# Kernel optimization log

Measured on AMD Instinct MI355X. Metric: run time of the kernel, lower is better.

## Reference

```python
import jax, jax.numpy as jnp
import numpy as np

S = 16384          # vision tokens (one image, 128x128 patches)
HID = 1280         # vision_hidden_size
H = 16             # num heads
D = HID // H       # head_dim = 80
L = 8              # vision_depth
FF = 3456          # vision_intermediate_size
WIN = 64           # tokens per attention window
UNIT = 4           # spatial_merge_size ** 2
OUT = 2048         # vision_out_hidden_size
PV = 3 * 2 * 16 * 16  # patch volume = 1536


def setup_inputs() -> dict:
    keys = iter(jax.random.split(jax.random.key(0), 32))
    def nrm(shape, fan_in):
        return jax.random.normal(next(keys), shape, jnp.float32) * (fan_in ** -0.5)
    ang = jax.random.uniform(next(keys), (S, D // 2), jnp.float32, 0.0, 2.0 * float(np.pi))
    ang = jnp.concatenate([ang, ang], axis=-1)  # rotate_half-compatible duplicated layout
    return {
        "x": jax.random.normal(next(keys), (S, PV), jnp.float32),
        "cos": jnp.cos(ang), "sin": jnp.sin(ang),
        "cu_seqlens": jnp.arange(S // WIN + 1, dtype=jnp.int32) * WIN,
        "pe_w": nrm((PV, HID), PV), "pe_b": jnp.zeros((HID,), jnp.float32),
        "ln1_w": jnp.ones((L, HID), jnp.float32), "ln1_b": jnp.zeros((L, HID), jnp.float32),
        "qkv_w": nrm((L, HID, 3 * HID), HID), "qkv_b": jnp.zeros((L, 3 * HID), jnp.float32),
        "proj_w": nrm((L, HID, HID), HID), "proj_b": jnp.zeros((L, HID), jnp.float32),
        "ln2_w": jnp.ones((L, HID), jnp.float32), "ln2_b": jnp.zeros((L, HID), jnp.float32),
        "fc1_w": nrm((L, HID, FF), HID), "fc1_b": jnp.zeros((L, FF), jnp.float32),
        "fc2_w": nrm((L, FF, HID), FF), "fc2_b": jnp.zeros((L, HID), jnp.float32),
        "m_ln_w": jnp.ones((HID,), jnp.float32), "m_ln_b": jnp.zeros((HID,), jnp.float32),
        "m_fc1_w": nrm((UNIT * HID, UNIT * HID), UNIT * HID), "m_fc1_b": jnp.zeros((UNIT * HID,), jnp.float32),
        "m_fc2_w": nrm((UNIT * HID, OUT), UNIT * HID), "m_fc2_b": jnp.zeros((OUT,), jnp.float32),
    }


def _ln(t, w, b, eps=1e-6):
    m = jnp.mean(t, axis=-1, keepdims=True)
    v = jnp.mean((t - m) ** 2, axis=-1, keepdims=True)
    return (t - m) * jax.lax.rsqrt(v + eps) * w + b


def _forward(cu_seqlens, x, cos, sin, pe_w, pe_b, ln1_w, ln1_b, qkv_w, qkv_b,
             proj_w, proj_b, ln2_w, ln2_b, fc1_w, fc1_b, fc2_w, fc2_b,
             m_ln_w, m_ln_b, m_fc1_w, m_fc1_b, m_fc2_w, m_fc2_b):
    NW = cu_seqlens.shape[0] - 1  # uniform windows (static)
    W = S // NW
    scale = D ** -0.5
    cosr = cos[:, None, :]  # [S,1,D]
    sinr = sin[:, None, :]

    def rope(t):  # t: [S,H,D]
        t1, t2 = jnp.split(t, 2, axis=-1)
        return t * cosr + jnp.concatenate((-t2, t1), axis=-1) * sinr

    h = x @ pe_w + pe_b  # patch embed: [S, HID]

    def block(h, p):
        l1w, l1b, qw, qb, pw, pb, l2w, l2b, f1w, f1b, f2w, f2b = p
        xn = _ln(h, l1w, l1b)
        q, k, v = jnp.split(xn @ qw + qb, 3, axis=-1)
        q = rope(q.reshape(S, H, D))
        k = rope(k.reshape(S, H, D))
        v = v.reshape(S, H, D)
        # block-diagonal (windowed) attention, fp32 scores as in source
        qw_ = q.reshape(NW, W, H, D)
        kw_ = k.reshape(NW, W, H, D)
        vw_ = v.reshape(NW, W, H, D)
        scores = jnp.einsum('wqhd,wkhd->whqk', qw_, kw_) * scale
        attn = jnp.einsum('whqk,wkhd->wqhd', jax.nn.softmax(scores, axis=-1), vw_)
        h = h + (attn.reshape(S, HID) @ pw + pb)
        xn2 = _ln(h, l2w, l2b)
        h = h + (jax.nn.gelu(xn2 @ f1w + f1b, approximate=True) @ f2w + f2b)
        return h, None

    h, _ = jax.lax.scan(block, h, (ln1_w, ln1_b, qkv_w, qkv_b, proj_w, proj_b,
                                   ln2_w, ln2_b, fc1_w, fc1_b, fc2_w, fc2_b))
    # patch merger (pre-shuffle norm)
    hm = _ln(h, m_ln_w, m_ln_b).reshape(-1, UNIT * HID)  # [S/4, 5120]
    return jax.nn.gelu(hm @ m_fc1_w + m_fc1_b, approximate=True) @ m_fc2_w + m_fc2_b


def reference(x, cos, sin, cu_seqlens, pe_w, pe_b, ln1_w, ln1_b, qkv_w, qkv_b,
              proj_w, proj_b, ln2_w, ln2_b, fc1_w, fc1_b, fc2_w, fc2_b,
              m_ln_w, m_ln_b, m_fc1_w, m_fc1_b, m_fc2_w, m_fc2_b):
    return _forward(cu_seqlens, x, cos, sin, pe_w, pe_b, ln1_w, ln1_b, qkv_w, qkv_b,
                    proj_w, proj_b, ln2_w, ln2_b, fc1_w, fc1_b, fc2_w, fc2_b,
                    m_ln_w, m_ln_b, m_fc1_w, m_fc1_b, m_fc2_w, m_fc2_b)
```

## Files before the change

kernel.cpp:

```cpp
#include <hip/hip_runtime.h>

typedef unsigned short ushortT;
typedef __attribute__((ext_vector_type(8))) short short8;
typedef __attribute__((ext_vector_type(8))) unsigned short ushort8;
typedef __attribute__((ext_vector_type(4))) unsigned short ushort4v;
typedef __attribute__((ext_vector_type(4))) float f32x4;

#define DEVINL __device__ __forceinline__

DEVINL ushortT f2bf(float f) {
    unsigned u = __builtin_bit_cast(unsigned, f);
    u += 0x7FFFu + ((u >> 16) & 1u);
    return (ushortT)(u >> 16);
}
DEVINL float bf2f(ushortT h) {
    unsigned u = ((unsigned)h) << 16;
    return __builtin_bit_cast(float, u);
}
DEVINL float gelu_tanh(float x) {
    float x3 = x * x * x;
    return 0.5f * x * (1.0f + tanhf(0.7978845608028654f * (x + 0.044715f * x3)));
}

#define GLOAD_LDS16(g, l)                                                     \
    __builtin_amdgcn_global_load_lds(                                         \
        (const __attribute__((address_space(1))) void*)(g),                   \
        (__attribute__((address_space(3))) void*)(l), 16, 0, 0)

#define WAITV(n) asm volatile("s_waitcnt vmcnt(" #n ")" ::: "memory")
#define MEMFENCE() asm volatile("" ::: "memory")
#define BAR() __builtin_amdgcn_s_barrier()
#define BARF() MEMFENCE(); BAR(); MEMFENCE()

__global__ __launch_bounds__(256) void cast_bf16_4(const float* __restrict__ in,
                                                   ushortT* __restrict__ out, long n4) {
    long i = (long)blockIdx.x * 256 + threadIdx.x;
    if (i < n4) {
        const float* p = in + i * 4;
        ushort4v o;
        o[0] = f2bf(p[0]); o[1] = f2bf(p[1]); o[2] = f2bf(p[2]); o[3] = f2bf(p[3]);
        ((ushort4v*)out)[i] = o;
    }
}

__global__ __launch_bounds__(256) void transpose_cast(const float* __restrict__ in,
                                                      ushortT* __restrict__ out,
                                                      int K, int N, int Npad) {
    __shared__ float tile[32][33];
    long zi = (long)blockIdx.z * K * N;
    long zo = (long)blockIdx.z * Npad * K;
    const float* ip = in + zi;
    ushortT* op = out + zo;
    int t = threadIdx.x, bx = blockIdx.x, by = blockIdx.y;
#pragma unroll
    for (int i = 0; i < 4; i++) {
        int idx = i * 256 + t, r = idx >> 5, c = idx & 31;
        int col = bx * 32 + c;
        tile[r][c] = (col < N) ? ip[(long)(by * 32 + r) * N + col] : 0.0f;
    }
    __syncthreads();
#pragma unroll
    for (int i = 0; i < 4; i++) {
        int idx = i * 256 + t, r = idx >> 5, c = idx & 31;
        op[(long)(bx * 32 + r) * K + by * 32 + c] = f2bf(tile[c][r]);
    }
}

__global__ __launch_bounds__(256) void pad_bias(const float* __restrict__ in,
                                                float* __restrict__ out,
                                                int n_in, int n_out, int total) {
    int i = blockIdx.x * 256 + threadIdx.x;
    if (i < total) {
        int l = i / n_out, c = i % n_out;
        out[i] = (c < n_in) ? in[l * n_in + c] : 0.0f;
    }
}

__global__ __launch_bounds__(256) void ln_to_bf16(const float* __restrict__ in,
                                                  const float* __restrict__ w,
                                                  const float* __restrict__ b,
                                                  ushortT* __restrict__ out) {
    const int row = blockIdx.x;
    const float* x = in + (long)row * 1280;
    __shared__ float red[4];
    float v[5];
    float s = 0.f;
#pragma unroll
    for (int i = 0; i < 5; i++) { v[i] = x[threadIdx.x + i * 256]; s += v[i]; }
#pragma unroll
    for (int o = 32; o > 0; o >>= 1) s += __shfl_xor(s, o);
    int wave = threadIdx.x >> 6;
    if ((threadIdx.x & 63) == 0) red[wave] = s;
    __syncthreads();
    float mean = (red[0] + red[1] + red[2] + red[3]) * (1.0f / 1280.0f);
    float q = 0.f;
#pragma unroll
    for (int i = 0; i < 5; i++) { float d = v[i] - mean; q += d * d; }
#pragma unroll
    for (int o = 32; o > 0; o >>= 1) q += __shfl_xor(q, o);
    __syncthreads();
    if ((threadIdx.x & 63) == 0) red[wave] = q;
    __syncthreads();
    float var = (red[0] + red[1] + red[2] + red[3]) * (1.0f / 1280.0f);
    float rs = rsqrtf(var + 1e-6f);
#pragma unroll
    for (int i = 0; i < 5; i++) {
        int c = threadIdx.x + i * 256;
        out[(long)row * 1280 + c] = f2bf((v[i] - mean) * rs * w[c] + b[c]);
    }
}


#define GSTAGE(mat, ls, base, ld, k0, buf)                                    \
    _Pragma("unroll") for (int j = 0; j < 2; j++) {                           \
        int c = j * 256 + t; int sr = c >> 2, sl = c & 3;                     \
        GLOAD_LDS16(mat + (base + sr) * ld + (k0) + ((sl ^ ((sr >> 1) & 3)) * 8), \
                    &ls[buf][c * 8]);                                         \
    }
#define GREAD()                                                               \
    _Pragma("unroll") for (int m = 0; m < 4; m++) {                           \
        int r = wr * 64 + m * 16 + lr;                                        \
        aF[m] = *(const short8*)&lsA[rbuf][r * 32 + ((lg ^ ((r >> 1) & 3)) * 8)]; \
    }                                                                         \
    _Pragma("unroll") for (int n = 0; n < 4; n++) {                           \
        int r = wc * 64 + n * 16 + lr;                                        \
        bF[n] = *(const short8*)&lsB[rbuf][r * 32 + ((lg ^ ((r >> 1) & 3)) * 8)]; \
    }
#define GMFMA()                                                               \
    __builtin_amdgcn_s_setprio(1);                                            \
    _Pragma("unroll") for (int m = 0; m < 4; m++)                             \
    _Pragma("unroll") for (int n = 0; n < 4; n++)                             \
        acc[m][n] = __builtin_amdgcn_mfma_f32_16x16x32_bf16(                  \
            aF[m], bF[n], acc[m][n], 0, 0, 0);                                \
    __builtin_amdgcn_s_setprio(0);

template <bool OBF, bool RES, bool GEL>
__global__ __launch_bounds__(256, 3)
void gemm_r3(const ushortT* __restrict__ A, const ushortT* __restrict__ Bt,
             const float* __restrict__ bias, const float* __restrict__ res,
             void* __restrict__ out, int M, int N, int K, int lda, int ldb) {
    __shared__ ushortT lsA[3][4096];
    __shared__ ushortT lsB[3][4096];
    const int t = threadIdx.x;
    const int lane = t & 63, lr = lane & 15, lg = lane >> 4;
    const int wave = t >> 6;
    const int wr = wave >> 1, wc = wave & 1;

    const int nwg = gridDim.x, orig = blockIdx.x;
    const int q = nwg >> 3, r8 = nwg & 7;
    const int xcd = orig & 7, loc = orig >> 3;
    const int wg = (xcd < r8 ? xcd * (q + 1) : r8 * (q + 1) + (xcd - r8) * q) + loc;
    const int gx = N >> 7;
    const size_t brow = (size_t)(wg / gx) * 128;
    const size_t bcol = (size_t)(wg % gx) * 128;

    f32x4 acc[4][4];
#pragma unroll
    for (int m = 0; m < 4; m++)
#pragma unroll
        for (int n = 0; n < 4; n++) acc[m][n] = f32x4{0.f, 0.f, 0.f, 0.f};

    GSTAGE(A, lsA, brow, lda, 0, 0);
    GSTAGE(Bt, lsB, bcol, ldb, 0, 0);
    GSTAGE(A, lsA, brow, lda, 32, 1);
    GSTAGE(Bt, lsB, bcol, ldb, 32, 1);
    WAITV(4); BARF();

    short8 aF[4], bF[4];
    const int NT = K >> 5;
    int tt = 0;
    for (; tt < NT - 2; ++tt) {
        const int rbuf = tt % 3, sbuf = (tt + 2) % 3;
        const int k2 = (tt + 2) << 5;
        MEMFENCE();
        GREAD();
        GSTAGE(A, lsA, brow, lda, k2, sbuf);
        GSTAGE(Bt, lsB, bcol, ldb, k2, sbuf);
        WAITV(4);
        BARF();
        GMFMA();
    }
    {
        const int rbuf = tt % 3;
        MEMFENCE();
        GREAD();
        WAITV(0);
        BARF();
        GMFMA();
        ++tt;
    }
    {
        const int rbuf = tt % 3;
        MEMFENCE();
        GREAD();
        GMFMA();
    }

#pragma unroll
    for (int m = 0; m < 4; m++) {
#pragma unroll
        for (int n = 0; n < 4; n++) {
#pragma unroll
            for (int rr = 0; rr < 4; rr++) {
                size_t row = brow + wr * 64 + m * 16 + lg * 4 + rr;
                size_t col = bcol + wc * 64 + n * 16 + lr;
                float v = acc[m][n][rr] + bias[col];
                if (RES) v += res[row * N + col];
                if (GEL) v = gelu_tanh(v);
                if (OBF) ((ushortT*)out)[row * N + col] = f2bf(v);
                else     ((float*)out)[row * N + col] = v;
            }
        }
    }
}

__global__ __launch_bounds__(256) void attn_win(const ushortT* __restrict__ qkv,
                                                const float* __restrict__ cosb,
                                                const float* __restrict__ sinb,
                                                ushortT* __restrict__ out) {
    const int w = blockIdx.x, h = blockIdx.y;
    __shared__ ushortT qs[64 * 96];
    __shared__ ushortT ks[64 * 96];
    __shared__ ushortT vt[80 * 80];
    __shared__ float   sc[64 * 65];
    __shared__ ushortT pb[64 * 80];
    const int t = threadIdx.x, wave = t >> 6, lane = t & 63, lr = lane & 15, lg = lane >> 4;
    const ushortT* bq = qkv + (long)w * 64 * 3840 + h * 80;

    for (int c = t; c < 640; c += 256) {
        int r = c / 10, cb = c % 10;
        const ushortT* qp = bq + (long)r * 3840;
        ushort8 qa = *(const ushort8*)(qp + cb * 8);
        ushort8 ka = *(const ushort8*)(qp + 1280 + cb * 8);
        int pcb = (cb < 5) ? cb + 5 : cb - 5;
        ushort8 qpr = *(const ushort8*)(qp + pcb * 8);
        ushort8 kpr = *(const ushort8*)(qp + 1280 + pcb * 8);
        long srow = (long)w * 64 + r;
        const float* cp = cosb + srow * 80 + cb * 8;
        const float* sp = sinb + srow * 80 + cb * 8;
        float sgn = (cb < 5) ? -1.f : 1.f;
        ushort8 qo, ko;
#pragma unroll
        for (int j = 0; j < 8; j++) {
            float c_ = cp[j], s_ = sp[j] * sgn;
            qo[j] = f2bf(bf2f(qa[j]) * c_ + bf2f(qpr[j]) * s_);
            ko[j] = f2bf(bf2f(ka[j]) * c_ + bf2f(kpr[j]) * s_);
        }
        *(ushort8*)&qs[r * 96 + cb * 8] = qo;
        *(ushort8*)&ks[r * 96 + cb * 8] = ko;
        ushort8 vv = *(const ushort8*)(qp + 2560 + cb * 8);
#pragma unroll
        for (int j = 0; j < 8; j++) vt[(cb * 8 + j) * 80 + r] = vv[j];
    }
    for (int idx = t; idx < 1024; idx += 256) {
        int r = idx >> 4, c2 = 80 + (idx & 15);
        qs[r * 96 + c2] = 0;
        ks[r * 96 + c2] = 0;
    }
    __syncthreads();

    f32x4 sa[4];
#pragma unroll
    for (int n = 0; n < 4; n++) sa[n] = f32x4{0.f, 0.f, 0.f, 0.f};
#pragma unroll
    for (int kk = 0; kk < 3; kk++) {
        short8 aq = *(const short8*)&qs[(wave * 16 + lr) * 96 + kk * 32 + lg * 8];
#pragma unroll
        for (int n = 0; n < 4; n++) {
            short8 bk = *(const short8*)&ks[(n * 16 + lr) * 96 + kk * 32 + lg * 8];
            sa[n] = __builtin_amdgcn_mfma_f32_16x16x32_bf16(aq, bk, sa[n], 0, 0, 0);
        }
    }
    const float scale = 0.11180339887498949f;
#pragma unroll
    for (int n = 0; n < 4; n++)
#pragma unroll
        for (int r = 0; r < 4; r++)
            sc[(wave * 16 + lg * 4 + r) * 65 + n * 16 + lr] = sa[n][r] * scale;
    __syncthreads();

    {
        int row = t >> 2, q4 = t & 3;
        float pv[16];
        float mx = -1e30f;
#pragma unroll
        for (int j = 0; j < 16; j++) { pv[j] = sc[row * 65 + q4 * 16 + j]; mx = fmaxf(mx, pv[j]); }
        mx = fmaxf(mx, __shfl_xor(mx, 1));
        mx = fmaxf(mx, __shfl_xor(mx, 2));
        float sum = 0.f;
#pragma unroll
        for (int j = 0; j < 16; j++) { pv[j] = __expf(pv[j] - mx); sum += pv[j]; }
        sum += __shfl_xor(sum, 1);
        sum += __shfl_xor(sum, 2);
        float inv = 1.0f / sum;
#pragma unroll
        for (int j = 0; j < 16; j++) pb[row * 80 + q4 * 16 + j] = f2bf(pv[j] * inv);
    }
    __syncthreads();

    f32x4 pa[5];
#pragma unroll
    for (int n = 0; n < 5; n++) pa[n] = f32x4{0.f, 0.f, 0.f, 0.f};
#pragma unroll
    for (int kk = 0; kk < 2; kk++) {
        short8 ap = *(const short8*)&pb[(wave * 16 + lr) * 80 + kk * 32 + lg * 8];
#pragma unroll
        for (int n = 0; n < 5; n++) {
            short8 bv = *(const short8*)&vt[(n * 16 + lr) * 80 + kk * 32 + lg * 8];
            pa[n] = __builtin_amdgcn_mfma_f32_16x16x32_bf16(ap, bv, pa[n], 0, 0, 0);
        }
    }
    ushortT* ob = out + (long)w * 64 * 1280 + h * 80;
#pragma unroll
    for (int n = 0; n < 5; n++)
#pragma unroll
        for (int r = 0; r < 4; r++)
            ob[(long)(wave * 16 + lg * 4 + r) * 1280 + n * 16 + lr] = f2bf(pa[n][r]);
}

extern "C" void kernel_launch(void* const* d_in, const int* in_sizes, int n_in,
                              void* d_out, int out_size, void* d_ws, size_t ws_size,
                              hipStream_t stream) {
    const float* x      = (const float*)d_in[0];
    const float* cosb   = (const float*)d_in[1];
    const float* sinb   = (const float*)d_in[2];
    const float* pe_w   = (const float*)d_in[4];
    const float* pe_b   = (const float*)d_in[5];
    const float* ln1_w  = (const float*)d_in[6];
    const float* ln1_b  = (const float*)d_in[7];
    const float* qkv_w  = (const float*)d_in[8];
    const float* qkv_b  = (const float*)d_in[9];
    const float* proj_w = (const float*)d_in[10];
    const float* proj_b = (const float*)d_in[11];
    const float* ln2_w  = (const float*)d_in[12];
    const float* ln2_b  = (const float*)d_in[13];
    const float* fc1_w  = (const float*)d_in[14];
    const float* fc1_b  = (const float*)d_in[15];
    const float* fc2_w  = (const float*)d_in[16];
    const float* fc2_b  = (const float*)d_in[17];
    const float* mln_w  = (const float*)d_in[18];
    const float* mln_b  = (const float*)d_in[19];
    const float* mfc1_w = (const float*)d_in[20];
    const float* mfc1_b = (const float*)d_in[21];
    const float* mfc2_w = (const float*)d_in[22];
    const float* mfc2_b = (const float*)d_in[23];

    char* ws = (char*)d_ws;
    size_t off = 0;
    auto alloc = [&](size_t bytes) -> char* {
        char* p = ws + off;
        off += (bytes + 255) & ~(size_t)255;
        return p;
    };
    ushortT* pe_wT   = (ushortT*)alloc((size_t)1280 * 1536 * 2);
    ushortT* qkv_wT  = (ushortT*)alloc((size_t)8 * 3840 * 1280 * 2);
    ushortT* proj_wT = (ushortT*)alloc((size_t)8 * 1280 * 1280 * 2);
    ushortT* fc1_wT  = (ushortT*)alloc((size_t)8 * 3584 * 1280 * 2);
    ushortT* fc2_wT  = (ushortT*)alloc((size_t)8 * 1280 * 3456 * 2);
    ushortT* mfc1_wT = (ushortT*)alloc((size_t)5120 * 5120 * 2);
    ushortT* mfc2_wT = (ushortT*)alloc((size_t)2048 * 5120 * 2);
    float*   fc1_bp  = (float*)alloc((size_t)8 * 3584 * 4);
    float*   hbuf    = (float*)alloc((size_t)16384 * 1280 * 4);
    ushortT* xn      = (ushortT*)alloc((size_t)16384 * 1280 * 2);
    ushortT* big     = (ushortT*)alloc((size_t)16384 * 3840 * 2);
    ushortT* attnb   = (ushortT*)alloc((size_t)16384 * 1280 * 2);

    ushortT* xbf  = big;
    ushortT* qkvb = big;
    ushortT* ffn1 = big;
    ushortT* t1   = attnb;

    transpose_cast<<<dim3(1280 / 32, 1536 / 32, 1), 256, 0, stream>>>(pe_w,   pe_wT,   1536, 1280, 1280);
    transpose_cast<<<dim3(3840 / 32, 1280 / 32, 8), 256, 0, stream>>>(qkv_w,  qkv_wT,  1280, 3840, 3840);
    transpose_cast<<<dim3(1280 / 32, 1280 / 32, 8), 256, 0, stream>>>(proj_w, proj_wT, 1280, 1280, 1280);
    transpose_cast<<<dim3(3584 / 32, 1280 / 32, 8), 256, 0, stream>>>(fc1_w,  fc1_wT,  1280, 3456, 3584);
    transpose_cast<<<dim3(1280 / 32, 3456 / 32, 8), 256, 0, stream>>>(fc2_w,  fc2_wT,  3456, 1280, 1280);
    transpose_cast<<<dim3(5120 / 32, 5120 / 32, 1), 256, 0, stream>>>(mfc1_w, mfc1_wT, 5120, 5120, 5120);
    transpose_cast<<<dim3(2048 / 32, 5120 / 32, 1), 256, 0, stream>>>(mfc2_w, mfc2_wT, 5120, 2048, 2048);
    pad_bias<<<(8 * 3584 + 255) / 256, 256, 0, stream>>>(fc1_b, fc1_bp, 3456, 3584, 8 * 3584);

    cast_bf16_4<<<(16384L * 1536 / 4 + 255) / 256, 256, 0, stream>>>(x, xbf, 16384L * 1536 / 4);
    gemm_r3<false, false, false><<<dim3(128 * 10), 256, 0, stream>>>(
        xbf, pe_wT, pe_b, nullptr, hbuf, 16384, 1280, 1536, 1536, 1536);

    for (int l = 0; l < 8; l++) {
        ln_to_bf16<<<16384, 256, 0, stream>>>(hbuf, ln1_w + l * 1280, ln1_b + l * 1280, xn);
        gemm_r3<true, false, false><<<dim3(128 * 30), 256, 0, stream>>>(
            xn, qkv_wT + (size_t)l * 3840 * 1280, qkv_b + l * 3840, nullptr, qkvb,
            16384, 3840, 1280, 1280, 1280);
        attn_win<<<dim3(256, 16), 256, 0, stream>>>(qkvb, cosb, sinb, attnb);
        gemm_r3<false, true, false><<<dim3(128 * 10), 256, 0, stream>>>(
            attnb, proj_wT + (size_t)l * 1280 * 1280, proj_b + l * 1280, hbuf, hbuf,
            16384, 1280, 1280, 1280, 1280);
        ln_to_bf16<<<16384, 256, 0, stream>>>(hbuf, ln2_w + l * 1280, ln2_b + l * 1280, xn);
        gemm_r3<true, false, true><<<dim3(128 * 28), 256, 0, stream>>>(
            xn, fc1_wT + (size_t)l * 3584 * 1280, fc1_bp + l * 3584, nullptr, ffn1,
            16384, 3584, 1280, 1280, 1280);
        gemm_r3<false, true, false><<<dim3(128 * 10), 256, 0, stream>>>(
            ffn1, fc2_wT + (size_t)l * 1280 * 3456, fc2_b + l * 1280, hbuf, hbuf,
            16384, 1280, 3456, 3584, 3456);
    }

    ln_to_bf16<<<16384, 256, 0, stream>>>(hbuf, mln_w, mln_b, xn);
    gemm_r3<true, false, true><<<dim3(32 * 40), 256, 0, stream>>>(
        xn, mfc1_wT, mfc1_b, nullptr, t1, 4096, 5120, 5120, 5120, 5120);
    gemm_r3<false, false, false><<<dim3(32 * 16), 256, 0, stream>>>(
        t1, mfc2_wT, mfc2_b, nullptr, (float*)d_out, 4096, 2048, 5120, 5120, 5120);
}
```

Before: 7.364 ms.

## Replace LDS-staged GEMM pipeline with direct global-to-register double-buffered loads

Drops the triple-buffered LDS staging (global_load_lds, barriers, swizzled reads) from the bf16 MFMA GEMM. Each wave now loads its A and B fragments straight from global memory into registers, alternating between two register buffers so loads overlap with MFMAs. This removes LDS traffic and block-wide barriers. In exchange it loses cross-wave operand sharing, so each A and B row is fetched by two waves, global accesses become narrow strided 64-byte row segments, and register pressure rises. The loop also assumes K/32 is even, which holds for every call here.

```diff
diff --git a/kernel.cpp b/kernel.cpp
--- a/kernel.cpp
+++ b/kernel.cpp
@@ -21,16 +21,6 @@
     float x3 = x * x * x;
     return 0.5f * x * (1.0f + tanhf(0.7978845608028654f * (x + 0.044715f * x3)));
 }
-
-#define GLOAD_LDS16(g, l)                                                     \
-    __builtin_amdgcn_global_load_lds(                                         \
-        (const __attribute__((address_space(1))) void*)(g),                   \
-        (__attribute__((address_space(3))) void*)(l), 16, 0, 0)
-
-#define WAITV(n) asm volatile("s_waitcnt vmcnt(" #n ")" ::: "memory")
-#define MEMFENCE() asm volatile("" ::: "memory")
-#define BAR() __builtin_amdgcn_s_barrier()
-#define BARF() MEMFENCE(); BAR(); MEMFENCE()
 
 __global__ __launch_bounds__(256) void cast_bf16_4(const float* __restrict__ in,
                                                    ushortT* __restrict__ out, long n4) {
@@ -111,36 +101,22 @@
 }
 
 
-#define GSTAGE(mat, ls, base, ld, k0, buf)                                    \
-    _Pragma("unroll") for (int j = 0; j < 2; j++) {                           \
-        int c = j * 256 + t; int sr = c >> 2, sl = c & 3;                     \
-        GLOAD_LDS16(mat + (base + sr) * ld + (k0) + ((sl ^ ((sr >> 1) & 3)) * 8), \
-                    &ls[buf][c * 8]);                                         \
-    }
-#define GREAD()                                                               \
-    _Pragma("unroll") for (int m = 0; m < 4; m++) {                           \
-        int r = wr * 64 + m * 16 + lr;                                        \
-        aF[m] = *(const short8*)&lsA[rbuf][r * 32 + ((lg ^ ((r >> 1) & 3)) * 8)]; \
-    }                                                                         \
-    _Pragma("unroll") for (int n = 0; n < 4; n++) {                           \
-        int r = wc * 64 + n * 16 + lr;                                        \
-        bF[n] = *(const short8*)&lsB[rbuf][r * 32 + ((lg ^ ((r >> 1) & 3)) * 8)]; \
-    }
-#define GMFMA()                                                               \
-    __builtin_amdgcn_s_setprio(1);                                            \
+#define LOADF(aa, bb, k)                                                      \
+    _Pragma("unroll") for (int m = 0; m < 4; m++)                             \
+        aa[m] = *(const short8*)(pA[m] + (k));                                \
+    _Pragma("unroll") for (int n = 0; n < 4; n++)                             \
+        bb[n] = *(const short8*)(pB[n] + (k));
+#define MM(aa, bb)                                                            \
     _Pragma("unroll") for (int m = 0; m < 4; m++)                             \
     _Pragma("unroll") for (int n = 0; n < 4; n++)                             \
         acc[m][n] = __builtin_amdgcn_mfma_f32_16x16x32_bf16(                  \
-            aF[m], bF[n], acc[m][n], 0, 0, 0);                                \
-    __builtin_amdgcn_s_setprio(0);
+            aa[m], bb[n], acc[m][n], 0, 0, 0);
 
 template <bool OBF, bool RES, bool GEL>
 __global__ __launch_bounds__(256, 3)
-void gemm_r3(const ushortT* __restrict__ A, const ushortT* __restrict__ Bt,
-             const float* __restrict__ bias, const float* __restrict__ res,
-             void* __restrict__ out, int M, int N, int K, int lda, int ldb) {
-    __shared__ ushortT lsA[3][4096];
-    __shared__ ushortT lsB[3][4096];
+void gemm_reg(const ushortT* __restrict__ A, const ushortT* __restrict__ Bt,
+              const float* __restrict__ bias, const float* __restrict__ res,
+              void* __restrict__ out, int M, int N, int K, int lda, int ldb) {
     const int t = threadIdx.x;
     const int lane = t & 63, lr = lane & 15, lg = lane >> 4;
     const int wave = t >> 6;
@@ -154,47 +130,34 @@
     const size_t brow = (size_t)(wg / gx) * 128;
     const size_t bcol = (size_t)(wg % gx) * 128;
 
+    const ushortT* pA[4];
+    const ushortT* pB[4];
+#pragma unroll
+    for (int m = 0; m < 4; m++)
+        pA[m] = A + (brow + wr * 64 + m * 16 + lr) * (size_t)lda + lg * 8;
+#pragma unroll
+    for (int n = 0; n < 4; n++)
+        pB[n] = Bt + (bcol + wc * 64 + n * 16 + lr) * (size_t)ldb + lg * 8;
+
     f32x4 acc[4][4];
 #pragma unroll
     for (int m = 0; m < 4; m++)
 #pragma unroll
         for (int n = 0; n < 4; n++) acc[m][n] = f32x4{0.f, 0.f, 0.f, 0.f};
 
-    GSTAGE(A, lsA, brow, lda, 0, 0);
-    GSTAGE(Bt, lsB, bcol, ldb, 0, 0);
-    GSTAGE(A, lsA, brow, lda, 32, 1);
-    GSTAGE(Bt, lsB, bcol, ldb, 32, 1);
-    WAITV(4); BARF();
-
-    short8 aF[4], bF[4];
-    const int NT = K >> 5;
-    int tt = 0;
-    for (; tt < NT - 2; ++tt) {
-        const int rbuf = tt % 3, sbuf = (tt + 2) % 3;
-        const int k2 = (tt + 2) << 5;
-        MEMFENCE();
-        GREAD();
-        GSTAGE(A, lsA, brow, lda, k2, sbuf);
-        GSTAGE(Bt, lsB, bcol, ldb, k2, sbuf);
-        WAITV(4);
-        BARF();
-        GMFMA();
-    }
-    {
-        const int rbuf = tt % 3;
-        MEMFENCE();
-        GREAD();
-        WAITV(0);
-        BARF();
-        GMFMA();
-        ++tt;
-    }
-    {
-        const int rbuf = tt % 3;
-        MEMFENCE();
-        GREAD();
-        GMFMA();
-    }
+    short8 a0[4], b0[4], a1[4], b1[4];
+    LOADF(a0, b0, 0);
+    const int KE = K - 32;
+    int k = 32;
+    for (; k < KE; k += 64) {
+        LOADF(a1, b1, k);
+        MM(a0, b0);
+        LOADF(a0, b0, k + 32);
+        MM(a1, b1);
+    }
+    LOADF(a1, b1, KE);
+    MM(a0, b0);
+    MM(a1, b1);
 
 #pragma unroll
     for (int m = 0; m < 4; m++) {
@@ -380,30 +343,30 @@
     pad_bias<<<(8 * 3584 + 255) / 256, 256, 0, stream>>>(fc1_b, fc1_bp, 3456, 3584, 8 * 3584);
 
     cast_bf16_4<<<(16384L * 1536 / 4 + 255) / 256, 256, 0, stream>>>(x, xbf, 16384L * 1536 / 4);
-    gemm_r3<false, false, false><<<dim3(128 * 10), 256, 0, stream>>>(
+    gemm_reg<false, false, false><<<dim3(128 * 10), 256, 0, stream>>>(
         xbf, pe_wT, pe_b, nullptr, hbuf, 16384, 1280, 1536, 1536, 1536);
 
     for (int l = 0; l < 8; l++) {
         ln_to_bf16<<<16384, 256, 0, stream>>>(hbuf, ln1_w + l * 1280, ln1_b + l * 1280, xn);
-        gemm_r3<true, false, false><<<dim3(128 * 30), 256, 0, stream>>>(
+        gemm_reg<true, false, false><<<dim3(128 * 30), 256, 0, stream>>>(
             xn, qkv_wT + (size_t)l * 3840 * 1280, qkv_b + l * 3840, nullptr, qkvb,
             16384, 3840, 1280, 1280, 1280);
         attn_win<<<dim3(256, 16), 256, 0, stream>>>(qkvb, cosb, sinb, attnb);
-        gemm_r3<false, true, false><<<dim3(128 * 10), 256, 0, stream>>>(
+        gemm_reg<false, true, false><<<dim3(128 * 10), 256, 0, stream>>>(
             attnb, proj_wT + (size_t)l * 1280 * 1280, proj_b + l * 1280, hbuf, hbuf,
             16384, 1280, 1280, 1280, 1280);
         ln_to_bf16<<<16384, 256, 0, stream>>>(hbuf, ln2_w + l * 1280, ln2_b + l * 1280, xn);
-        gemm_r3<true, false, true><<<dim3(128 * 28), 256, 0, stream>>>(
+        gemm_reg<true, false, true><<<dim3(128 * 28), 256, 0, stream>>>(
             xn, fc1_wT + (size_t)l * 3584 * 1280, fc1_bp + l * 3584, nullptr, ffn1,
             16384, 3584, 1280, 1280, 1280);
-        gemm_r3<false, true, false><<<dim3(128 * 10), 256, 0, stream>>>(
+        gemm_reg<false, true, false><<<dim3(128 * 10), 256, 0, stream>>>(
             ffn1, fc2_wT + (size_t)l * 1280 * 3456, fc2_b + l * 1280, hbuf, hbuf,
             16384, 1280, 3456, 3584, 3456);
     }
 
     ln_to_bf16<<<16384, 256, 0, stream>>>(hbuf, mln_w, mln_b, xn);
-    gemm_r3<true, false, true><<<dim3(32 * 40), 256, 0, stream>>>(
+    gemm_reg<true, false, true><<<dim3(32 * 40), 256, 0, stream>>>(
         xn, mfc1_wT, mfc1_b, nullptr, t1, 4096, 5120, 5120, 5120, 5120);
-    gemm_r3<false, false, false><<<dim3(32 * 16), 256, 0, stream>>>(
+    gemm_reg<false, false, false><<<dim3(32 * 16), 256, 0, stream>>>(
         t1, mfc2_wT, mfc2_b, nullptr, (float*)d_out, 4096, 2048, 5120, 5120, 5120);
 }
```

Result: slower. 16.42 ms (+123.0%).
